# Optimization experiments

Measured on AMD Instinct MI355X. Metric: run time of the kernel, lower is better.

The kernel has to match this reference:

```python
import jax, jax.numpy as jnp
import numpy as np

NUM_HEADS = 16
HEAD_DIM = 64
EMB = 1024


def setup_inputs() -> dict:
    key = jax.random.key(0)
    k1, k2, k3 = jax.random.split(key, 3)
    x = jax.random.normal(k1, (4, 1024, EMB), dtype=jnp.float32)
    W_qkv = jax.random.normal(k2, (EMB, 3 * NUM_HEADS * HEAD_DIM), dtype=jnp.float32) * (EMB ** -0.5)
    b_qkv = jnp.zeros((3 * NUM_HEADS * HEAD_DIM,), dtype=jnp.float32)
    W_out = jax.random.normal(k3, (NUM_HEADS * HEAD_DIM, EMB), dtype=jnp.float32) * ((NUM_HEADS * HEAD_DIM) ** -0.5)
    b_out = jnp.zeros((EMB,), dtype=jnp.float32)
    return {"x": x, "W_qkv": W_qkv, "b_qkv": b_qkv, "W_out": W_out, "b_out": b_out}


def reference(x, W_qkv, b_qkv, W_out, b_out):
    B, N, D = x.shape
    qkv = x @ W_qkv + b_qkv                      # B N 3*H*hd
    # torch.split order in the source is K, Q, V
    K, Q, V = jnp.split(qkv, 3, axis=-1)
    def heads(t):  # B N (H hd) -> B H N hd
        return t.reshape(B, N, NUM_HEADS, HEAD_DIM).transpose(0, 2, 1, 3)
    K, Q, V = heads(K), heads(Q), heads(V)
    scores = jnp.einsum('bhqd,bhkd->bhqk', Q, K) / (HEAD_DIM ** 0.5)
    att = jax.nn.softmax(scores, axis=-1)        # dropout p=0.0 -> identity
    out = jnp.einsum('bhqk,bhkd->bhqd', att, V)  # B H N hd
    out = out.transpose(0, 2, 1, 3).reshape(B, N, NUM_HEADS * HEAD_DIM)
    return out @ W_out + b_out
```

## Files before the change

kernel.cpp:

```cpp
#include <hip/hip_runtime.h>
#include <hip/hip_bf16.h>
#include <cstddef>
#include <cmath>


typedef _Float16 f16x4 __attribute__((ext_vector_type(4)));
typedef _Float16 f16x8 __attribute__((ext_vector_type(8)));
typedef float    f32x4 __attribute__((ext_vector_type(4)));

#define LOG2E 1.4426950408889634f

__device__ __forceinline__ void gload_lds16(const void* g, void* l) {
    __builtin_amdgcn_global_load_lds(
        (const __attribute__((address_space(1))) unsigned int*)g,
        (__attribute__((address_space(3))) unsigned int*)l, 16, 0, 0);
}

__global__ __launch_bounds__(256) void cvt_f32_f16(
    const float* __restrict__ in, _Float16* __restrict__ out, int n8)
{
    int i = blockIdx.x * 256 + threadIdx.x;
    if (i < n8) {
        const float4* p = (const float4*)in;
        float4 v0 = p[i * 2], v1 = p[i * 2 + 1];
        f16x8 o;
        o[0] = (_Float16)v0.x; o[1] = (_Float16)v0.y; o[2] = (_Float16)v0.z; o[3] = (_Float16)v0.w;
        o[4] = (_Float16)v1.x; o[5] = (_Float16)v1.y; o[6] = (_Float16)v1.z; o[7] = (_Float16)v1.w;
        *(f16x8*)(out + (size_t)i * 8) = o;
    }
}

__global__ __launch_bounds__(256) void transpose_f32_to_f16(
    const float* __restrict__ in, _Float16* __restrict__ out, int R, int C)
{
    __shared__ float tile[64][65];
    int r0 = blockIdx.y * 64, c0 = blockIdx.x * 64;
    int t = threadIdx.x;
#pragma unroll
    for (int p = 0; p < 4; ++p) {
        int lin = p * 256 + t;
        int row = lin >> 4;
        int c4 = (lin & 15) * 4;
        float4 v = *(const float4*)(in + (size_t)(r0 + row) * C + c0 + c4);
        tile[row][c4] = v.x; tile[row][c4 + 1] = v.y;
        tile[row][c4 + 2] = v.z; tile[row][c4 + 3] = v.w;
    }
    __syncthreads();
#pragma unroll
    for (int p = 0; p < 2; ++p) {
        int lin = p * 256 + t;
        int oc = lin >> 3;
        int ch = (lin & 7) * 8;
        f16x8 o;
#pragma unroll
        for (int e = 0; e < 8; ++e) o[e] = (_Float16)tile[ch + e][oc];
        *(f16x8*)(out + (size_t)(c0 + oc) * R + r0 + ch) = o;
    }
}

__global__ __launch_bounds__(256) void transpose_f16(
    const _Float16* __restrict__ in, _Float16* __restrict__ out, int R, int C)
{
    __shared__ _Float16 tile[64][72];
    const _Float16* inh = in + (size_t)blockIdx.z * R * C;
    _Float16* outh = out + (size_t)blockIdx.z * R * C;
    int r0 = blockIdx.y * 64, c0 = blockIdx.x * 64;
    int t = threadIdx.x;
#pragma unroll
    for (int p = 0; p < 2; ++p) {
        int lin = p * 256 + t;
        int row = lin >> 3;
        int ch = (lin & 7) * 8;
        f16x8 v = *(const f16x8*)(inh + (size_t)(r0 + row) * C + c0 + ch);
        *(f16x8*)&tile[row][ch] = v;
    }
    __syncthreads();
#pragma unroll
    for (int p = 0; p < 2; ++p) {
        int lin = p * 256 + t;
        int oc = lin >> 3;
        int ch = (lin & 7) * 8;
        f16x8 o;
#pragma unroll
        for (int e = 0; e < 8; ++e) o[e] = tile[ch + e][oc];
        *(f16x8*)(outh + (size_t)(c0 + oc) * R + r0 + ch) = o;
    }
}

template <int EPI>
__global__ __launch_bounds__(256) void gemm_f16(
    const _Float16* __restrict__ A, const _Float16* __restrict__ Bt,
    const float* __restrict__ bias, float* __restrict__ Cout,
    _Float16* __restrict__ Kh, _Float16* __restrict__ Qh, _Float16* __restrict__ Vh,
    int M, int Nn, int Kk)
{
    __shared__ _Float16 As[2][128 * 64];
    __shared__ _Float16 Bs[2][128 * 64];

    int lin = blockIdx.y * gridDim.x + blockIdx.x;
    int nwg = gridDim.x * gridDim.y;
    int lin2 = (lin & 7) * (nwg >> 3) + (lin >> 3);
    int bx = lin2 % gridDim.x, by = lin2 / gridDim.x;
    int m0 = by * 128, n0 = bx * 128;

    int t = threadIdx.x, lane = t & 63, wid = t >> 6;
    int wr = (wid >> 1) * 64, wc = (wid & 1) * 64;
    int lr = lane & 15, lg = lane >> 4;

    f32x4 acc[4][4] = {};
    int nt = Kk >> 6;

#pragma unroll
    for (int p = 0; p < 4; ++p) {
        int c = p * 256 + t;
        int row = c >> 3, col = (c & 7) * 8;
        int ubase = (p * 256 + wid * 64) * 8;
        gload_lds16(A  + (size_t)(m0 + row) * Kk + col, &As[0][ubase]);
        gload_lds16(Bt + (size_t)(n0 + row) * Kk + col, &Bs[0][ubase]);
    }
    __syncthreads();

    for (int tt = 0; tt < nt; ++tt) {
        int cur = tt & 1;
        if (tt + 1 < nt) {
            int k0 = (tt + 1) * 64;
#pragma unroll
            for (int p = 0; p < 4; ++p) {
                int c = p * 256 + t;
                int row = c >> 3, col = (c & 7) * 8;
                int ubase = (p * 256 + wid * 64) * 8;
                gload_lds16(A  + (size_t)(m0 + row) * Kk + k0 + col, &As[cur ^ 1][ubase]);
                gload_lds16(Bt + (size_t)(n0 + row) * Kk + k0 + col, &Bs[cur ^ 1][ubase]);
            }
        }
        const _Float16* Ac = &As[cur][0];
        const _Float16* Bc = &Bs[cur][0];
#pragma unroll
        for (int kk = 0; kk < 2; ++kk) {
            f16x8 af[4], bfr[4];
#pragma unroll
            for (int i = 0; i < 4; ++i) {
                af[i]  = *(const f16x8*)&Ac[(wr + i * 16 + lr) * 64 + kk * 32 + lg * 8];
                bfr[i] = *(const f16x8*)&Bc[(wc + i * 16 + lr) * 64 + kk * 32 + lg * 8];
            }
#pragma unroll
            for (int i = 0; i < 4; ++i)
#pragma unroll
                for (int jn = 0; jn < 4; ++jn)
                    acc[i][jn] = __builtin_amdgcn_mfma_f32_16x16x32_f16(
                        af[i], bfr[jn], acc[i][jn], 0, 0, 0);
        }
        __syncthreads();
    }

#pragma unroll
    for (int i = 0; i < 4; ++i)
#pragma unroll
        for (int jn = 0; jn < 4; ++jn) {
            int gc = n0 + wc + jn * 16 + lr;
            float bv = bias[gc];
#pragma unroll
            for (int j = 0; j < 4; ++j) {
                int gr = m0 + wr + i * 16 + lg * 4 + j;
                float v = acc[i][jn][j] + bv;
                if constexpr (EPI == 0) {
                    Cout[(size_t)gr * Nn + gc] = v;
                } else {
                    int sec = gc >> 10, idx = gc & 1023;
                    int h = idx >> 6, d = idx & 63;
                    int bb = gr >> 10, pos = gr & 1023;
                    size_t hoff = (((size_t)(bb * 16 + h) * 1024) + pos) * 64 + d;
                    if (sec == 0)      Kh[hoff] = (_Float16)v;
                    else if (sec == 1) Qh[hoff] = (_Float16)(v * (0.125f * LOG2E));
                    else               Vh[hoff] = (_Float16)v;
                }
            }
        }
}

__global__ __launch_bounds__(256) void attn_kernel(
    const _Float16* __restrict__ Qh, const _Float16* __restrict__ Kh,
    const _Float16* __restrict__ Vt, _Float16* __restrict__ attO)
{
    __shared__ _Float16 Ks[2][64 * 64];
    __shared__ _Float16 Vs[2][64 * 64];
    __shared__ _Float16 Pl[4][16 * 64];

    int wg = blockIdx.x;
    int swz = (wg & 7) * 128 + (wg >> 3);
    int bh = swz >> 4, qt = swz & 15;
    int b = bh >> 4, h = bh & 15;

    int tid = threadIdx.x;
    int wid = tid >> 6, lane = tid & 63;
    int lr = lane & 15, lg = lane >> 4;
    int q0 = qt * 64 + wid * 16;
    const _Float16* Qb = Qh + (size_t)bh * (1024 * 64);
    const _Float16* Kb = Kh + (size_t)bh * (1024 * 64);
    const _Float16* Vb = Vt + (size_t)bh * (64 * 1024);

    int c0 = tid, c1 = 256 + tid;
    int r0 = c0 >> 3, sc0 = ((c0 & 7) * 16) ^ ((r0 & 7) << 4);
    int r1 = c1 >> 3, sc1 = ((c1 & 7) * 16) ^ ((r1 & 7) << 4);
    int ub0 = (wid * 64) * 8, ub1 = (256 + wid * 64) * 8;

    f16x8 qf0 = *(const f16x8*)(Qb + (size_t)(q0 + lr) * 64 + lg * 8);
    f16x8 qf1 = *(const f16x8*)(Qb + (size_t)(q0 + lr) * 64 + 32 + lg * 8);

    float m = -1e30f, l = 0.f;
    f32x4 o[4] = {};
    int xr = (lr & 7) << 4;

    gload_lds16(Kb + (size_t)r0 * 64 + (sc0 >> 1), &Ks[0][ub0]);
    gload_lds16(Kb + (size_t)r1 * 64 + (sc1 >> 1), &Ks[0][ub1]);
    gload_lds16(Vb + (size_t)r0 * 1024 + (sc0 >> 1), &Vs[0][ub0]);
    gload_lds16(Vb + (size_t)r1 * 1024 + (sc1 >> 1), &Vs[0][ub1]);
    __syncthreads();

    for (int t = 0; t < 16; ++t) {
        int cur = t & 1;
        if (t < 15) {
            int kn = (t + 1) * 64;
            gload_lds16(Kb + (size_t)(kn + r0) * 64 + (sc0 >> 1), &Ks[cur ^ 1][ub0]);
            gload_lds16(Kb + (size_t)(kn + r1) * 64 + (sc1 >> 1), &Ks[cur ^ 1][ub1]);
            gload_lds16(Vb + (size_t)r0 * 1024 + kn + (sc0 >> 1), &Vs[cur ^ 1][ub0]);
            gload_lds16(Vb + (size_t)r1 * 1024 + kn + (sc1 >> 1), &Vs[cur ^ 1][ub1]);
        }
        const _Float16* Kc = &Ks[cur][0];
        const _Float16* Vc = &Vs[cur][0];

        f32x4 s[4] = {};
#pragma unroll
        for (int kb = 0; kb < 4; ++kb) {
            const char* krow = (const char*)(Kc + (kb * 16 + lr) * 64);
            f16x8 kf0 = *(const f16x8*)(krow + ((lg * 16) ^ xr));
            f16x8 kf1 = *(const f16x8*)(krow + ((64 + lg * 16) ^ xr));
            s[kb] = __builtin_amdgcn_mfma_f32_16x16x32_f16(kf0, qf0, s[kb], 0, 0, 0);
            s[kb] = __builtin_amdgcn_mfma_f32_16x16x32_f16(kf1, qf1, s[kb], 0, 0, 0);
        }
        float a0 = fmaxf(fmaxf(s[0][0], s[0][1]), fmaxf(s[0][2], s[0][3]));
        float a1 = fmaxf(fmaxf(s[1][0], s[1][1]), fmaxf(s[1][2], s[1][3]));
        float a2 = fmaxf(fmaxf(s[2][0], s[2][1]), fmaxf(s[2][2], s[2][3]));
        float a3 = fmaxf(fmaxf(s[3][0], s[3][1]), fmaxf(s[3][2], s[3][3]));
        float pmax = fmaxf(fmaxf(a0, a1), fmaxf(a2, a3));
        pmax = fmaxf(pmax, __shfl_xor(pmax, 16));
        pmax = fmaxf(pmax, __shfl_xor(pmax, 32));
        float mnew = fmaxf(m, pmax);
        float corr = exp2f(m - mnew);
#pragma unroll
        for (int kb = 0; kb < 4; ++kb)
#pragma unroll
            for (int j = 0; j < 4; ++j)
                s[kb][j] = exp2f(s[kb][j] - mnew);
        float rr0 = (s[0][0] + s[0][1]) + (s[0][2] + s[0][3]);
        float rr1 = (s[1][0] + s[1][1]) + (s[1][2] + s[1][3]);
        float rr2 = (s[2][0] + s[2][1]) + (s[2][2] + s[2][3]);
        float rr3 = (s[3][0] + s[3][1]) + (s[3][2] + s[3][3]);
        float rs = (rr0 + rr1) + (rr2 + rr3);
        rs += __shfl_xor(rs, 16);
        rs += __shfl_xor(rs, 32);
        l = l * corr + rs;
        m = mnew;
#pragma unroll
        for (int db = 0; db < 4; ++db)
#pragma unroll
            for (int j = 0; j < 4; ++j) o[db][j] *= corr;

        char* prow = (char*)&Pl[wid][lr * 64];
#pragma unroll
        for (int kb = 0; kb < 4; ++kb) {
            f16x4 w;
#pragma unroll
            for (int j = 0; j < 4; ++j) w[j] = (_Float16)s[kb][j];
            *(f16x4*)(prow + ((kb * 32 + lg * 8) ^ xr)) = w;
        }
        f16x8 pf0 = *(const f16x8*)(prow + ((lg * 16) ^ xr));
        f16x8 pf1 = *(const f16x8*)(prow + ((64 + lg * 16) ^ xr));

#pragma unroll
        for (int db = 0; db < 4; ++db) {
            const char* vrow = (const char*)(Vc + (db * 16 + lr) * 64);
            f16x8 vf0 = *(const f16x8*)(vrow + ((lg * 16) ^ xr));
            f16x8 vf1 = *(const f16x8*)(vrow + ((64 + lg * 16) ^ xr));
            o[db] = __builtin_amdgcn_mfma_f32_16x16x32_f16(vf0, pf0, o[db], 0, 0, 0);
            o[db] = __builtin_amdgcn_mfma_f32_16x16x32_f16(vf1, pf1, o[db], 0, 0, 0);
        }
        __syncthreads();
    }

    float li = 1.f / l;
#pragma unroll
    for (int db = 0; db < 4; ++db) {
        f16x4 w;
#pragma unroll
        for (int j = 0; j < 4; ++j) w[j] = (_Float16)(o[db][j] * li);
        *(f16x4*)(attO + ((size_t)b * 1024 + q0 + lr) * 1024 + h * 64 + db * 16 + lg * 4) = w;
    }
}

extern "C" void kernel_launch(void* const* d_in, const int* in_sizes, int n_in,
                              void* d_out, int out_size, void* d_ws, size_t ws_size,
                              hipStream_t stream)
{
    const float* x    = (const float*)d_in[0];
    const float* Wqkv = (const float*)d_in[1];
    const float* bqkv = (const float*)d_in[2];
    const float* Wout = (const float*)d_in[3];
    const float* bout = (const float*)d_in[4];
    float* out = (float*)d_out;

    char* ws = (char*)d_ws;
    _Float16* xb    = (_Float16*)(ws);
    _Float16* Vt    = (_Float16*)(ws);
    _Float16* Wqkvt = (_Float16*)(ws + ((size_t)8  << 20));
    _Float16* Woutt = (_Float16*)(ws + ((size_t)14 << 20));
    _Float16* Qh    = (_Float16*)(ws + ((size_t)16 << 20));
    _Float16* Kh    = (_Float16*)(ws + ((size_t)24 << 20));
    _Float16* Vh    = (_Float16*)(ws + ((size_t)32 << 20));
    _Float16* attO  = (_Float16*)(ws + ((size_t)40 << 20));

    cvt_f32_f16<<<2048, 256, 0, stream>>>(x, xb, 4096 * 1024 / 8);
    transpose_f32_to_f16<<<dim3(48, 16), 256, 0, stream>>>(Wqkv, Wqkvt, 1024, 3072);
    transpose_f32_to_f16<<<dim3(16, 16), 256, 0, stream>>>(Wout, Woutt, 1024, 1024);

    gemm_f16<1><<<dim3(24, 32), 256, 0, stream>>>(
        xb, Wqkvt, bqkv, nullptr, Kh, Qh, Vh, 4096, 3072, 1024);

    transpose_f16<<<dim3(1, 16, 64), 256, 0, stream>>>(Vh, Vt, 1024, 64);

    attn_kernel<<<1024, 256, 0, stream>>>(Qh, Kh, Vt, attO);

    gemm_f16<0><<<dim3(8, 32), 256, 0, stream>>>(
        attO, Woutt, bout, out, nullptr, nullptr, nullptr, 4096, 1024, 1024);
}
```

Measured before the change: 211.3 us.

## Use 256x256 tile GEMM with triple-buffered LDS for QKV projection

Adds a new GEMM kernel with 256x256 output tiles, 512 threads, a K-step of 32 and a three-stage direct-to-LDS load pipeline using XOR-swizzled shared memory. The QKV projection uses it instead of the 128x128 kernel. The larger tile raises arithmetic intensity and cuts global loads per FLOP, and loads for upcoming stages are interleaved with MFMA work under raised priority. The grid drops to 192 workgroups, which underfills the 256 CUs on this GPU and may leave many idle. The large accumulator count also increases register pressure.

Result: faster. 190.9 us (-9.6%).

```diff
diff --git a/kernel.cpp b/kernel.cpp
--- a/kernel.cpp
+++ b/kernel.cpp
@@ -85,6 +85,124 @@
         for (int e = 0; e < 8; ++e) o[e] = tile[ch + e][oc];
         *(f16x8*)(outh + (size_t)(c0 + oc) * R + r0 + ch) = o;
     }
+}
+
+template <int EPI>
+__global__ __launch_bounds__(512, 2) void gemm256(
+    const _Float16* __restrict__ A, const _Float16* __restrict__ Bt,
+    const float* __restrict__ bias, float* __restrict__ Cout,
+    _Float16* __restrict__ Kh, _Float16* __restrict__ Qh, _Float16* __restrict__ Vh,
+    int M, int Nn, int Kk)
+{
+    __shared__ _Float16 As[3][256 * 32];
+    __shared__ _Float16 Bs[3][256 * 32];
+
+    int lin = blockIdx.y * gridDim.x + blockIdx.x;
+    int nwg = gridDim.x * gridDim.y;
+    int lin2 = (lin & 7) * (nwg >> 3) + (lin >> 3);
+    int bx = lin2 % gridDim.x, by = lin2 / gridDim.x;
+    int m0 = by * 256, n0 = bx * 256;
+
+    int tid = threadIdx.x, lane = tid & 63, wid = tid >> 6;
+    int wm = wid >> 2, wn = wid & 3;
+    int lr = lane & 15, lg = lane >> 4;
+
+    int srow = tid >> 2;
+    int scol = ((tid & 3) * 8) ^ ((srow & 6) << 2);
+    const _Float16* pa0 = A  + (size_t)(m0 + srow) * Kk + scol;
+    const _Float16* pa1 = A  + (size_t)(m0 + 128 + srow) * Kk + scol;
+    const _Float16* pb0 = Bt + (size_t)(n0 + srow) * Kk + scol;
+    const _Float16* pb1 = Bt + (size_t)(n0 + 128 + srow) * Kk + scol;
+    int d0 = (wid * 64) * 8;
+    int d1 = (512 + wid * 64) * 8;
+
+    f32x4 acc[8][4] = {};
+    const int NIT = Kk >> 5;
+
+    {
+        gload_lds16(pa0, &As[0][d0]); gload_lds16(pa1, &As[0][d1]);
+        gload_lds16(pb0, &Bs[0][d0]); gload_lds16(pb1, &Bs[0][d1]);
+        gload_lds16(pa0 + 32, &As[1][d0]); gload_lds16(pa1 + 32, &As[1][d1]);
+        gload_lds16(pb0 + 32, &Bs[1][d0]); gload_lds16(pb1 + 32, &Bs[1][d1]);
+    }
+
+    for (int i = 0; i < NIT; ++i) {
+        const _Float16* Ab = &As[i % 3][0];
+        const _Float16* Bb = &Bs[i % 3][0];
+        int sb = (i + 2) % 3;
+        int ks = (i + 2 < NIT) ? (i + 2) * 32 : 0;
+
+        asm volatile("s_waitcnt vmcnt(4)" ::: "memory");
+        __builtin_amdgcn_s_barrier();
+
+        f16x8 bf[4], af[4];
+#pragma unroll
+        for (int nf = 0; nf < 4; ++nf) {
+            int rn = wn * 64 + nf * 16 + lr;
+            bf[nf] = *(const f16x8*)&Bb[rn * 32 + ((lg * 8) ^ ((rn & 6) << 2))];
+        }
+#pragma unroll
+        for (int mf = 0; mf < 4; ++mf) {
+            int ra = wm * 128 + mf * 16 + lr;
+            af[mf] = *(const f16x8*)&Ab[ra * 32 + ((lg * 8) ^ ((ra & 6) << 2))];
+        }
+        gload_lds16(pa0 + ks, &As[sb][d0]);
+        gload_lds16(pa1 + ks, &As[sb][d1]);
+        asm volatile("s_waitcnt lgkmcnt(0)" ::: "memory");
+        __builtin_amdgcn_sched_barrier(0);
+        __builtin_amdgcn_s_setprio(1);
+#pragma unroll
+        for (int mf = 0; mf < 4; ++mf)
+#pragma unroll
+            for (int nf = 0; nf < 4; ++nf)
+                acc[mf][nf] = __builtin_amdgcn_mfma_f32_16x16x32_f16(
+                    af[mf], bf[nf], acc[mf][nf], 0, 0, 0);
+        __builtin_amdgcn_s_setprio(0);
+
+#pragma unroll
+        for (int mf = 0; mf < 4; ++mf) {
+            int ra = wm * 128 + 64 + mf * 16 + lr;
+            af[mf] = *(const f16x8*)&Ab[ra * 32 + ((lg * 8) ^ ((ra & 6) << 2))];
+        }
+        gload_lds16(pb0 + ks, &Bs[sb][d0]);
+        gload_lds16(pb1 + ks, &Bs[sb][d1]);
+        asm volatile("s_waitcnt lgkmcnt(0)" ::: "memory");
+        __builtin_amdgcn_sched_barrier(0);
+        __builtin_amdgcn_s_setprio(1);
+#pragma unroll
+        for (int mf = 0; mf < 4; ++mf)
+#pragma unroll
+            for (int nf = 0; nf < 4; ++nf)
+                acc[4 + mf][nf] = __builtin_amdgcn_mfma_f32_16x16x32_f16(
+                    af[mf], bf[nf], acc[4 + mf][nf], 0, 0, 0);
+        __builtin_amdgcn_s_setprio(0);
+    }
+
+#pragma unroll
+    for (int mh = 0; mh < 2; ++mh)
+#pragma unroll
+        for (int mf = 0; mf < 4; ++mf)
+#pragma unroll
+            for (int nf = 0; nf < 4; ++nf) {
+                int gc = n0 + wn * 64 + nf * 16 + lr;
+                float bv = bias[gc];
+#pragma unroll
+                for (int j = 0; j < 4; ++j) {
+                    int gr = m0 + wm * 128 + mh * 64 + mf * 16 + lg * 4 + j;
+                    float v = acc[mh * 4 + mf][nf][j] + bv;
+                    if constexpr (EPI == 0) {
+                        Cout[(size_t)gr * Nn + gc] = v;
+                    } else {
+                        int sec = gc >> 10, idx = gc & 1023;
+                        int h = idx >> 6, d = idx & 63;
+                        int bb = gr >> 10, pos = gr & 1023;
+                        size_t hoff = (((size_t)(bb * 16 + h) * 1024) + pos) * 64 + d;
+                        if (sec == 0)      Kh[hoff] = (_Float16)v;
+                        else if (sec == 1) Qh[hoff] = (_Float16)(v * (0.125f * LOG2E));
+                        else               Vh[hoff] = (_Float16)v;
+                    }
+                }
+            }
 }
 
 template <int EPI>
@@ -323,7 +441,7 @@
     transpose_f32_to_f16<<<dim3(48, 16), 256, 0, stream>>>(Wqkv, Wqkvt, 1024, 3072);
     transpose_f32_to_f16<<<dim3(16, 16), 256, 0, stream>>>(Wout, Woutt, 1024, 1024);
 
-    gemm_f16<1><<<dim3(24, 32), 256, 0, stream>>>(
+    gemm256<1><<<dim3(12, 16), 512, 0, stream>>>(
         xb, Wqkvt, bqkv, nullptr, Kh, Qh, Vh, 4096, 3072, 1024);
 
     transpose_f16<<<dim3(1, 16, 64), 256, 0, stream>>>(Vh, Vt, 1024, 64);
```
